# Performance work log

Hardware: AMD Instinct MI355X
Metric: run time of the kernel (lower is better)

## Reference

```python
import jax, jax.numpy as jnp
import numpy as np

N_NODES = 100000


def _gcn_conv(x, W, b, src, dst, deg_inv_sqrt):
    # linear transform first (PyG GCNConv order): [N, F] @ [F, H]
    h = x @ W
    # symmetric normalization per edge: deg^-1/2[src] * deg^-1/2[dst]
    norm = deg_inv_sqrt[src] * deg_inv_sqrt[dst]
    msg = h[src] * norm[:, None]  # [E, H]
    out = jax.ops.segment_sum(msg, dst, num_segments=N_NODES)
    return out + b


def setup_inputs() -> dict:
    key = jax.random.key(0)
    k1, k2, k3, k4 = jax.random.split(key, 4)
    F_IN, H = 512, 512
    E = 800000
    x = jax.random.normal(k1, (N_NODES, F_IN), dtype=jnp.float32)
    edge_index = jax.random.randint(k2, (2, E), 0, N_NODES, dtype=jnp.int64)
    W1 = jax.random.normal(k3, (F_IN, H), dtype=jnp.float32) * (1.0 / np.sqrt(F_IN))
    b1 = jnp.zeros((H,), dtype=jnp.float32)
    W2 = jax.random.normal(k4, (H, H), dtype=jnp.float32) * (1.0 / np.sqrt(H))
    b2 = jnp.zeros((H,), dtype=jnp.float32)
    return {"x": x, "edge_index": edge_index, "W1": W1, "b1": b1, "W2": W2, "b2": b2}


def reference(x, edge_index, W1, b1, W2, b2):
    # add self loops (PyG GCNConv default add_self_loops=True)
    loop = jnp.arange(N_NODES, dtype=edge_index.dtype)
    src = jnp.concatenate([edge_index[0], loop])
    dst = jnp.concatenate([edge_index[1], loop])
    # degree of destination nodes (including self loops)
    deg = jax.ops.segment_sum(jnp.ones_like(dst, dtype=x.dtype), dst, num_segments=N_NODES)
    deg_inv_sqrt = jnp.where(deg > 0, jax.lax.rsqrt(jnp.maximum(deg, 1.0)), 0.0)
    h = jax.nn.relu(_gcn_conv(x, W1, b1, src, dst, deg_inv_sqrt))
    # dropout is identity at inference (training=False)
    out = _gcn_conv(h, W2, b2, src, dst, deg_inv_sqrt)
    return out
```

## Files before the change

kernel.cpp:

```cpp
#include <hip/hip_runtime.h>

#define N_NODES 100000
#define E_EDGES 800000
#define E_TOT   900000
#define F 512

typedef __attribute__((ext_vector_type(8))) short short8;
typedef __attribute__((ext_vector_type(4))) float f32x4;
typedef unsigned int u32;

__device__ __forceinline__ float bfu(unsigned int u) {
    union { unsigned int i; float f; } c; c.i = u << 16; return c.f;
}
__device__ __forceinline__ unsigned short f2b(float f) {
    union { float f; unsigned int u; } c; c.f = f;
    return (unsigned short)((c.u + 0x7fffu + ((c.u >> 16) & 1u)) >> 16);
}
__device__ __forceinline__ float fbits(unsigned int u) {
    union { unsigned int i; float f; } c; c.i = u; return c.f;
}
__device__ __forceinline__ unsigned int bits(float f) {
    union { float f; unsigned int i; } c; c.f = f; return c.i;
}
__device__ __forceinline__ void gload_lds16(const void* g, void* l) {
    __builtin_amdgcn_global_load_lds(
        (const __attribute__((address_space(1))) u32*)g,
        (__attribute__((address_space(3))) u32*)l, 16, 0, 0);
}

__global__ void k_init(unsigned int* deg, unsigned int* counter) {
    int i = blockIdx.x * 256 + threadIdx.x;
    if (i < N_NODES) deg[i] = 1u;
    if (i == 0) *counter = 0u;
}

__global__ void k_hist(const int* __restrict__ ei, unsigned int* deg) {
    int e = blockIdx.x * 256 + threadIdx.x;
    if (e < E_EDGES) atomicAdd(&deg[ei[E_EDGES + e]], 1u);
}

__global__ void k_disalloc(const unsigned int* __restrict__ deg, unsigned int* counter,
                           float* __restrict__ dis,
                           int2* __restrict__ seg, unsigned int* __restrict__ cursor) {
    int i = blockIdx.x * 256 + threadIdx.x;
    if (i < N_NODES) {
        unsigned int d = deg[i];
        dis[i] = rsqrtf((float)d);
        unsigned int p = atomicAdd(counter, d);
        seg[i] = make_int2((int)p, (int)(p + d));
        cursor[i] = p;
    }
}

__global__ void k_scatter(const int* __restrict__ ei, const float* __restrict__ dis,
                          unsigned int* __restrict__ cursor,
                          uint2* __restrict__ ev) {
    int e = blockIdx.x * 256 + threadIdx.x;
    if (e < E_TOT) {
        int s, d;
        if (e < E_EDGES) { s = ei[e]; d = ei[E_EDGES + e]; }
        else             { s = e - E_EDGES; d = s; }
        unsigned int p = atomicAdd(&cursor[d], 1u);
        ev[p] = make_uint2((unsigned)s, bits(dis[s] * dis[d]));
    }
}

__global__ void k_cvtX(const float* __restrict__ xin, unsigned short* __restrict__ xb) {
    int i = blockIdx.x * 256 + threadIdx.x;
    const f32x4* p = (const f32x4*)xin + (size_t)i * 2;
    f32x4 a = __builtin_nontemporal_load(p);
    f32x4 b = __builtin_nontemporal_load(p + 1);
    uint4 o;
    o.x = (unsigned)f2b(a[0]) | ((unsigned)f2b(a[1]) << 16);
    o.y = (unsigned)f2b(a[2]) | ((unsigned)f2b(a[3]) << 16);
    o.z = (unsigned)f2b(b[0]) | ((unsigned)f2b(b[1]) << 16);
    o.w = (unsigned)f2b(b[2]) | ((unsigned)f2b(b[3]) << 16);
    *(uint4*)(xb + (size_t)i * 8) = o;
}

__global__ void k_cvtW(const float* __restrict__ W1, const float* __restrict__ W2,
                       unsigned short* __restrict__ W1t, unsigned short* __restrict__ W2t) {
    int t = blockIdx.x * 256 + threadIdx.x;
    int which = t >= F * F;
    int u = t - which * F * F;
    int n = u >> 9, k = u & 511;
    const float* W = which ? W2 : W1;
    unsigned short* Wt = which ? W2t : W1t;
    Wt[u] = f2b(W[k * F + n]);
}

__global__ __launch_bounds__(512, 2)
void gemm_bt(const unsigned short* __restrict__ A, const unsigned short* __restrict__ Bt,
             const float* __restrict__ bias,
             unsigned short* __restrict__ outb, float* __restrict__ outf,
             int relu, int M) {
    __shared__ unsigned short sm[65536];

    int nwg = gridDim.x * gridDim.y;
    int orig = blockIdx.y * gridDim.x + blockIdx.x;
    int q = nwg >> 3, r = nwg & 7;
    int xcd = orig & 7, j8 = orig >> 3;
    int wgid = (xcd < r ? xcd * (q + 1) : r * (q + 1) + (xcd - r) * q) + j8;
    int by = wgid & 1;
    int bx = wgid >> 1;

    int t  = threadIdx.x;
    int lane = t & 63, w = t >> 6;
    int wr = w >> 2, wc = w & 3;
    int rsel = lane & 15, khalf = (lane >> 4) * 8;

    f32x4 acc[8][4];
    #pragma unroll
    for (int m = 0; m < 8; ++m)
        #pragma unroll
        for (int n = 0; n < 4; ++n)
            acc[m][n] = (f32x4){0.f, 0.f, 0.f, 0.f};

    int rowBase = bx * 256;

    int ar[4], br[4], kcc[4];
    #pragma unroll
    for (int i = 0; i < 4; ++i) {
        int idx = i * 512 + t;
        int rr = idx >> 3;
        kcc[i] = (idx & 7) * 8;
        int ga = rowBase + rr; if (ga >= M) ga = M - 1;
        ar[i] = ga;
        br[i] = by * 256 + rr;
    }

    auto STAGE = [&](int buf, int k0) {
        #pragma unroll
        for (int i = 0; i < 4; ++i) {
            int idx = i * 512 + t;
            gload_lds16(A + (size_t)ar[i] * F + k0 + kcc[i], sm + buf * 16384 + idx * 8);
            gload_lds16(Bt + (size_t)br[i] * F + k0 + kcc[i], sm + 32768 + buf * 16384 + idx * 8);
        }
    };
    auto COMPUTE = [&](int buf) {
        const unsigned short* la = sm + buf * 16384;
        const unsigned short* lb = sm + 32768 + buf * 16384;
        #pragma unroll
        for (int ks = 0; ks < 2; ++ks) {
            int koff = ks * 32 + khalf;
            short8 af[8], bfr[4];
            #pragma unroll
            for (int m = 0; m < 8; ++m)
                af[m] = *(const short8*)&la[(wr * 128 + m * 16 + rsel) * 64 + koff];
            #pragma unroll
            for (int n = 0; n < 4; ++n)
                bfr[n] = *(const short8*)&lb[(wc * 64 + n * 16 + rsel) * 64 + koff];
            #pragma unroll
            for (int m = 0; m < 8; ++m)
                #pragma unroll
                for (int n = 0; n < 4; ++n)
                    acc[m][n] = __builtin_amdgcn_mfma_f32_16x16x32_bf16(af[m], bfr[n], acc[m][n], 0, 0, 0);
        }
    };

    STAGE(0, 0);
    __syncthreads();
    #pragma unroll
    for (int kp = 0; kp < 4; ++kp) {
        STAGE(1, (2 * kp + 1) * 64);
        COMPUTE(0);
        __syncthreads();
        if (kp < 3) STAGE(0, (2 * kp + 2) * 64);
        COMPUTE(1);
        __syncthreads();
    }

    int rq = (lane >> 4) * 4, cq = lane & 15;
    if (outb) {
        #pragma unroll
        for (int m = 0; m < 8; ++m)
            #pragma unroll
            for (int n = 0; n < 4; ++n) {
                int cl = wc * 64 + n * 16 + cq;
                float bv = bias[by * 256 + cl];
                #pragma unroll
                for (int j = 0; j < 4; ++j) {
                    int rl = wr * 128 + m * 16 + rq + j;
                    float v = acc[m][n][j] + bv;
                    if (relu) v = fmaxf(v, 0.f);
                    sm[rl * 256 + cl] = f2b(v);
                }
            }
        __syncthreads();
        #pragma unroll
        for (int p = 0; p < 16; ++p) {
            int sidx = p * 4096 + t * 8;
            int row = sidx >> 8;
            int col = sidx & 255;
            int grow = rowBase + row;
            if (grow < M) {
                uint4 v = *(const uint4*)&sm[sidx];
                *(uint4*)&outb[(size_t)grow * F + by * 256 + col] = v;
            }
        }
    } else {
        #pragma unroll
        for (int m = 0; m < 8; ++m)
            #pragma unroll
            for (int n = 0; n < 4; ++n) {
                int colv = by * 256 + wc * 64 + n * 16 + cq;
                float bv = bias[colv];
                #pragma unroll
                for (int j = 0; j < 4; ++j) {
                    int row = rowBase + wr * 128 + m * 16 + rq + j;
                    if (row < M) {
                        float v = acc[m][n][j] + bv;
                        if (relu) v = fmaxf(v, 0.f);
                        __builtin_nontemporal_store(v, outf + (size_t)row * F + colv);
                    }
                }
            }
    }
}

__global__ __launch_bounds__(256)
void k_agg(const unsigned short* __restrict__ hin, const int2* __restrict__ seg,
           const uint2* __restrict__ ev,
           unsigned short* __restrict__ outb) {
    int node = blockIdx.x * 4 + (threadIdx.x >> 6);
    int lane = threadIdx.x & 63;
    if (node >= N_NODES) return;
    int2 se = seg[node];
    int e0 = se.x, e1 = se.y;
    float acc[8] = {0, 0, 0, 0, 0, 0, 0, 0};
    const unsigned short* base = hin + lane * 8;

    int e = e0;
    int n8 = e0 + ((e1 - e0) & ~7);
    for (; e < n8; e += 8) {
        uint2 p0 = ev[e],     p1 = ev[e + 1], p2 = ev[e + 2], p3 = ev[e + 3];
        uint2 p4 = ev[e + 4], p5 = ev[e + 5], p6 = ev[e + 6], p7 = ev[e + 7];
        uint4 v0 = *(const uint4*)(base + ((size_t)p0.x << 9));
        uint4 v1 = *(const uint4*)(base + ((size_t)p1.x << 9));
        uint4 v2 = *(const uint4*)(base + ((size_t)p2.x << 9));
        uint4 v3 = *(const uint4*)(base + ((size_t)p3.x << 9));
        uint4 v4 = *(const uint4*)(base + ((size_t)p4.x << 9));
        uint4 v5 = *(const uint4*)(base + ((size_t)p5.x << 9));
        uint4 v6 = *(const uint4*)(base + ((size_t)p6.x << 9));
        uint4 v7 = *(const uint4*)(base + ((size_t)p7.x << 9));
        float w0 = fbits(p0.y), w1 = fbits(p1.y), w2 = fbits(p2.y), w3 = fbits(p3.y);
        float w4 = fbits(p4.y), w5 = fbits(p5.y), w6 = fbits(p6.y), w7 = fbits(p7.y);
        acc[0] += w0 * bfu(v0.x & 0xffffu); acc[1] += w0 * bfu(v0.x >> 16);
        acc[2] += w0 * bfu(v0.y & 0xffffu); acc[3] += w0 * bfu(v0.y >> 16);
        acc[4] += w0 * bfu(v0.z & 0xffffu); acc[5] += w0 * bfu(v0.z >> 16);
        acc[6] += w0 * bfu(v0.w & 0xffffu); acc[7] += w0 * bfu(v0.w >> 16);
        acc[0] += w1 * bfu(v1.x & 0xffffu); acc[1] += w1 * bfu(v1.x >> 16);
        acc[2] += w1 * bfu(v1.y & 0xffffu); acc[3] += w1 * bfu(v1.y >> 16);
        acc[4] += w1 * bfu(v1.z & 0xffffu); acc[5] += w1 * bfu(v1.z >> 16);
        acc[6] += w1 * bfu(v1.w & 0xffffu); acc[7] += w1 * bfu(v1.w >> 16);
        acc[0] += w2 * bfu(v2.x & 0xffffu); acc[1] += w2 * bfu(v2.x >> 16);
        acc[2] += w2 * bfu(v2.y & 0xffffu); acc[3] += w2 * bfu(v2.y >> 16);
        acc[4] += w2 * bfu(v2.z & 0xffffu); acc[5] += w2 * bfu(v2.z >> 16);
        acc[6] += w2 * bfu(v2.w & 0xffffu); acc[7] += w2 * bfu(v2.w >> 16);
        acc[0] += w3 * bfu(v3.x & 0xffffu); acc[1] += w3 * bfu(v3.x >> 16);
        acc[2] += w3 * bfu(v3.y & 0xffffu); acc[3] += w3 * bfu(v3.y >> 16);
        acc[4] += w3 * bfu(v3.z & 0xffffu); acc[5] += w3 * bfu(v3.z >> 16);
        acc[6] += w3 * bfu(v3.w & 0xffffu); acc[7] += w3 * bfu(v3.w >> 16);
        acc[0] += w4 * bfu(v4.x & 0xffffu); acc[1] += w4 * bfu(v4.x >> 16);
        acc[2] += w4 * bfu(v4.y & 0xffffu); acc[3] += w4 * bfu(v4.y >> 16);
        acc[4] += w4 * bfu(v4.z & 0xffffu); acc[5] += w4 * bfu(v4.z >> 16);
        acc[6] += w4 * bfu(v4.w & 0xffffu); acc[7] += w4 * bfu(v4.w >> 16);
        acc[0] += w5 * bfu(v5.x & 0xffffu); acc[1] += w5 * bfu(v5.x >> 16);
        acc[2] += w5 * bfu(v5.y & 0xffffu); acc[3] += w5 * bfu(v5.y >> 16);
        acc[4] += w5 * bfu(v5.z & 0xffffu); acc[5] += w5 * bfu(v5.z >> 16);
        acc[6] += w5 * bfu(v5.w & 0xffffu); acc[7] += w5 * bfu(v5.w >> 16);
        acc[0] += w6 * bfu(v6.x & 0xffffu); acc[1] += w6 * bfu(v6.x >> 16);
        acc[2] += w6 * bfu(v6.y & 0xffffu); acc[3] += w6 * bfu(v6.y >> 16);
        acc[4] += w6 * bfu(v6.z & 0xffffu); acc[5] += w6 * bfu(v6.z >> 16);
        acc[6] += w6 * bfu(v6.w & 0xffffu); acc[7] += w6 * bfu(v6.w >> 16);
        acc[0] += w7 * bfu(v7.x & 0xffffu); acc[1] += w7 * bfu(v7.x >> 16);
        acc[2] += w7 * bfu(v7.y & 0xffffu); acc[3] += w7 * bfu(v7.y >> 16);
        acc[4] += w7 * bfu(v7.z & 0xffffu); acc[5] += w7 * bfu(v7.z >> 16);
        acc[6] += w7 * bfu(v7.w & 0xffffu); acc[7] += w7 * bfu(v7.w >> 16);
    }
    for (; e < e1; ++e) {
        uint2 p = ev[e];
        uint4 v = *(const uint4*)(base + ((size_t)p.x << 9));
        float wv = fbits(p.y);
        acc[0] += wv * bfu(v.x & 0xffffu); acc[1] += wv * bfu(v.x >> 16);
        acc[2] += wv * bfu(v.y & 0xffffu); acc[3] += wv * bfu(v.y >> 16);
        acc[4] += wv * bfu(v.z & 0xffffu); acc[5] += wv * bfu(v.z >> 16);
        acc[6] += wv * bfu(v.w & 0xffffu); acc[7] += wv * bfu(v.w >> 16);
    }

    uint4 o;
    o.x = (unsigned)f2b(acc[0]) | ((unsigned)f2b(acc[1]) << 16);
    o.y = (unsigned)f2b(acc[2]) | ((unsigned)f2b(acc[3]) << 16);
    o.z = (unsigned)f2b(acc[4]) | ((unsigned)f2b(acc[5]) << 16);
    o.w = (unsigned)f2b(acc[6]) | ((unsigned)f2b(acc[7]) << 16);
    *(uint4*)(outb + (size_t)node * F + lane * 8) = o;
}

extern "C" void kernel_launch(void* const* d_in, const int* in_sizes, int n_in,
                              void* d_out, int out_size, void* d_ws, size_t ws_size,
                              hipStream_t stream) {
    const float* x  = (const float*)d_in[0];
    const int*   ei = (const int*)d_in[1];
    const float* W1 = (const float*)d_in[2];
    const float* b1 = (const float*)d_in[3];
    const float* W2 = (const float*)d_in[4];
    const float* b2 = (const float*)d_in[5];
    float* out = (float*)d_out;

    char* ws = (char*)d_ws;
    size_t off = 0;
    auto alloc = [&](size_t bytes) -> void* {
        off = (off + 255) & ~(size_t)255;
        void* p = ws + off;
        off += bytes;
        return p;
    };

    unsigned short* tb  = (unsigned short*)alloc((size_t)N_NODES * F * 2);
    unsigned short* W1t = (unsigned short*)alloc((size_t)F * F * 2);
    unsigned short* W2t = (unsigned short*)alloc((size_t)F * F * 2);
    unsigned int*   deg = (unsigned int*)alloc((size_t)N_NODES * 4);
    float*          dis = (float*)alloc((size_t)N_NODES * 4);
    int2*           seg = (int2*)alloc((size_t)N_NODES * 8);
    unsigned int*   cur = (unsigned int*)alloc((size_t)N_NODES * 4);
    unsigned int*   cnt = (unsigned int*)alloc(256);
    uint2*          ev  = (uint2*)alloc((size_t)E_TOT * 8);

    unsigned short* h1b = (unsigned short*)d_out;
    unsigned short* xb  = (unsigned short*)((char*)d_out + (size_t)N_NODES * F * 2);

    int nb = (N_NODES + 255) / 256;

    k_init<<<nb, 256, 0, stream>>>(deg, cnt);
    k_hist<<<(E_EDGES + 255) / 256, 256, 0, stream>>>(ei, deg);
    k_disalloc<<<nb, 256, 0, stream>>>(deg, cnt, dis, seg, cur);
    k_scatter<<<(E_TOT + 255) / 256, 256, 0, stream>>>(ei, dis, cur, ev);

    k_cvtW<<<(2 * F * F) / 256, 256, 0, stream>>>(W1, W2, W1t, W2t);
    k_cvtX<<<(N_NODES * F / 8) / 256, 256, 0, stream>>>(x, xb);

    dim3 ggrid(2, (N_NODES + 255) / 256);

    k_agg<<<(N_NODES + 3) / 4, 256, 0, stream>>>(xb, seg, ev, tb);
    gemm_bt<<<ggrid, 512, 0, stream>>>(tb, W1t, b1, h1b, nullptr, 1, N_NODES);

    k_agg<<<(N_NODES + 3) / 4, 256, 0, stream>>>(h1b, seg, ev, tb);
    gemm_bt<<<ggrid, 512, 0, stream>>>(tb, W2t, b2, nullptr, out, 0, N_NODES);
}
```

Baseline: 647.3 us.

## Bucket each node's CSR edges by source-node chunk to improve gather locality

```diff
diff --git a/kernel.cpp b/kernel.cpp
--- a/kernel.cpp
+++ b/kernel.cpp
@@ -4,6 +4,8 @@
 #define E_EDGES 800000
 #define E_TOT   900000
 #define F 512
+#define NCHUNK 4
+#define CHUNK_SZ 25000
 
 typedef __attribute__((ext_vector_type(8))) short short8;
 typedef __attribute__((ext_vector_type(4))) float f32x4;
@@ -28,39 +30,50 @@
         (__attribute__((address_space(3))) u32*)l, 16, 0, 0);
 }
 
-__global__ void k_init(unsigned int* deg, unsigned int* counter) {
-    int i = blockIdx.x * 256 + threadIdx.x;
-    if (i < N_NODES) deg[i] = 1u;
-    if (i == 0) *counter = 0u;
-}
-
-__global__ void k_hist(const int* __restrict__ ei, unsigned int* deg) {
-    int e = blockIdx.x * 256 + threadIdx.x;
-    if (e < E_EDGES) atomicAdd(&deg[ei[E_EDGES + e]], 1u);
-}
-
-__global__ void k_disalloc(const unsigned int* __restrict__ deg, unsigned int* counter,
-                           float* __restrict__ dis,
-                           int2* __restrict__ seg, unsigned int* __restrict__ cursor) {
+__global__ void k_init(uint4* deg4, unsigned int* counter) {
     int i = blockIdx.x * 256 + threadIdx.x;
     if (i < N_NODES) {
-        unsigned int d = deg[i];
-        dis[i] = rsqrtf((float)d);
-        unsigned int p = atomicAdd(counter, d);
-        seg[i] = make_int2((int)p, (int)(p + d));
-        cursor[i] = p;
+        deg4[i] = make_uint4(0u, 0u, 0u, 0u);
+        ((unsigned int*)deg4)[i * 4 + i / CHUNK_SZ] = 1u;
+    }
+    if (i == 0) *counter = 0u;
+}
+
+__global__ void k_hist(const int* __restrict__ ei, unsigned int* deg4u) {
+    int e = blockIdx.x * 256 + threadIdx.x;
+    if (e < E_EDGES) {
+        int s = ei[e], d = ei[E_EDGES + e];
+        atomicAdd(&deg4u[(size_t)d * 4 + s / CHUNK_SZ], 1u);
+    }
+}
+
+__global__ void k_disalloc(uint4* deg4, unsigned int* counter,
+                           float* __restrict__ dis,
+                           int2* __restrict__ seg, int4* __restrict__ cst) {
+    int i = blockIdx.x * 256 + threadIdx.x;
+    if (i < N_NODES) {
+        uint4 d4 = deg4[i];
+        unsigned int tot = d4.x + d4.y + d4.z + d4.w;
+        dis[i] = rsqrtf((float)tot);
+        unsigned int p = atomicAdd(counter, tot);
+        int4 cs = make_int4((int)p, (int)(p + d4.x),
+                            (int)(p + d4.x + d4.y), (int)(p + d4.x + d4.y + d4.z));
+        cst[i] = cs;
+        seg[i] = make_int2((int)p, (int)(p + tot));
+        deg4[i] = make_uint4((unsigned)cs.x, (unsigned)cs.y,
+                             (unsigned)cs.z, (unsigned)cs.w);
     }
 }
 
 __global__ void k_scatter(const int* __restrict__ ei, const float* __restrict__ dis,
-                          unsigned int* __restrict__ cursor,
+                          unsigned int* __restrict__ cur4,
                           uint2* __restrict__ ev) {
     int e = blockIdx.x * 256 + threadIdx.x;
     if (e < E_TOT) {
         int s, d;
         if (e < E_EDGES) { s = ei[e]; d = ei[E_EDGES + e]; }
         else             { s = e - E_EDGES; d = s; }
-        unsigned int p = atomicAdd(&cursor[d], 1u);
+        unsigned int p = atomicAdd(&cur4[(size_t)d * 4 + s / CHUNK_SZ], 1u);
         ev[p] = make_uint2((unsigned)s, bits(dis[s] * dis[d]));
     }
 }
@@ -218,74 +231,38 @@
     }
 }
 
+#define LOADP(k) uint2 p##k = ev[e + k]
+#define LOADV(k) uint4 v##k = *(const uint4*)(base + ((size_t)p##k.x << 9))
+#define ACCV(k)  { float w_ = fbits(p##k.y); \
+    acc[0] += w_ * bfu(v##k.x & 0xffffu); acc[1] += w_ * bfu(v##k.x >> 16); \
+    acc[2] += w_ * bfu(v##k.y & 0xffffu); acc[3] += w_ * bfu(v##k.y >> 16); \
+    acc[4] += w_ * bfu(v##k.z & 0xffffu); acc[5] += w_ * bfu(v##k.z >> 16); \
+    acc[6] += w_ * bfu(v##k.w & 0xffffu); acc[7] += w_ * bfu(v##k.w >> 16); }
+
 __global__ __launch_bounds__(256)
 void k_agg(const unsigned short* __restrict__ hin, const int2* __restrict__ seg,
-           const uint2* __restrict__ ev,
+           const int4* __restrict__ cst, const uint2* __restrict__ ev,
            unsigned short* __restrict__ outb) {
     int node = blockIdx.x * 4 + (threadIdx.x >> 6);
     int lane = threadIdx.x & 63;
     if (node >= N_NODES) return;
     int2 se = seg[node];
-    int e0 = se.x, e1 = se.y;
+    int4 cs = cst[node];
+    int st[5] = {cs.x, cs.y, cs.z, cs.w, se.y};
     float acc[8] = {0, 0, 0, 0, 0, 0, 0, 0};
     const unsigned short* base = hin + lane * 8;
 
-    int e = e0;
-    int n8 = e0 + ((e1 - e0) & ~7);
-    for (; e < n8; e += 8) {
-        uint2 p0 = ev[e],     p1 = ev[e + 1], p2 = ev[e + 2], p3 = ev[e + 3];
-        uint2 p4 = ev[e + 4], p5 = ev[e + 5], p6 = ev[e + 6], p7 = ev[e + 7];
-        uint4 v0 = *(const uint4*)(base + ((size_t)p0.x << 9));
-        uint4 v1 = *(const uint4*)(base + ((size_t)p1.x << 9));
-        uint4 v2 = *(const uint4*)(base + ((size_t)p2.x << 9));
-        uint4 v3 = *(const uint4*)(base + ((size_t)p3.x << 9));
-        uint4 v4 = *(const uint4*)(base + ((size_t)p4.x << 9));
-        uint4 v5 = *(const uint4*)(base + ((size_t)p5.x << 9));
-        uint4 v6 = *(const uint4*)(base + ((size_t)p6.x << 9));
-        uint4 v7 = *(const uint4*)(base + ((size_t)p7.x << 9));
-        float w0 = fbits(p0.y), w1 = fbits(p1.y), w2 = fbits(p2.y), w3 = fbits(p3.y);
-        float w4 = fbits(p4.y), w5 = fbits(p5.y), w6 = fbits(p6.y), w7 = fbits(p7.y);
-        acc[0] += w0 * bfu(v0.x & 0xffffu); acc[1] += w0 * bfu(v0.x >> 16);
-        acc[2] += w0 * bfu(v0.y & 0xffffu); acc[3] += w0 * bfu(v0.y >> 16);
-        acc[4] += w0 * bfu(v0.z & 0xffffu); acc[5] += w0 * bfu(v0.z >> 16);
-        acc[6] += w0 * bfu(v0.w & 0xffffu); acc[7] += w0 * bfu(v0.w >> 16);
-        acc[0] += w1 * bfu(v1.x & 0xffffu); acc[1] += w1 * bfu(v1.x >> 16);
-        acc[2] += w1 * bfu(v1.y & 0xffffu); acc[3] += w1 * bfu(v1.y >> 16);
-        acc[4] += w1 * bfu(v1.z & 0xffffu); acc[5] += w1 * bfu(v1.z >> 16);
-        acc[6] += w1 * bfu(v1.w & 0xffffu); acc[7] += w1 * bfu(v1.w >> 16);
-        acc[0] += w2 * bfu(v2.x & 0xffffu); acc[1] += w2 * bfu(v2.x >> 16);
-        acc[2] += w2 * bfu(v2.y & 0xffffu); acc[3] += w2 * bfu(v2.y >> 16);
-        acc[4] += w2 * bfu(v2.z & 0xffffu); acc[5] += w2 * bfu(v2.z >> 16);
-        acc[6] += w2 * bfu(v2.w & 0xffffu); acc[7] += w2 * bfu(v2.w >> 16);
-        acc[0] += w3 * bfu(v3.x & 0xffffu); acc[1] += w3 * bfu(v3.x >> 16);
-        acc[2] += w3 * bfu(v3.y & 0xffffu); acc[3] += w3 * bfu(v3.y >> 16);
-        acc[4] += w3 * bfu(v3.z & 0xffffu); acc[5] += w3 * bfu(v3.z >> 16);
-        acc[6] += w3 * bfu(v3.w & 0xffffu); acc[7] += w3 * bfu(v3.w >> 16);
-        acc[0] += w4 * bfu(v4.x & 0xffffu); acc[1] += w4 * bfu(v4.x >> 16);
-        acc[2] += w4 * bfu(v4.y & 0xffffu); acc[3] += w4 * bfu(v4.y >> 16);
-        acc[4] += w4 * bfu(v4.z & 0xffffu); acc[5] += w4 * bfu(v4.z >> 16);
-        acc[6] += w4 * bfu(v4.w & 0xffffu); acc[7] += w4 * bfu(v4.w >> 16);
-        acc[0] += w5 * bfu(v5.x & 0xffffu); acc[1] += w5 * bfu(v5.x >> 16);
-        acc[2] += w5 * bfu(v5.y & 0xffffu); acc[3] += w5 * bfu(v5.y >> 16);
-        acc[4] += w5 * bfu(v5.z & 0xffffu); acc[5] += w5 * bfu(v5.z >> 16);
-        acc[6] += w5 * bfu(v5.w & 0xffffu); acc[7] += w5 * bfu(v5.w >> 16);
-        acc[0] += w6 * bfu(v6.x & 0xffffu); acc[1] += w6 * bfu(v6.x >> 16);
-        acc[2] += w6 * bfu(v6.y & 0xffffu); acc[3] += w6 * bfu(v6.y >> 16);
-        acc[4] += w6 * bfu(v6.z & 0xffffu); acc[5] += w6 * bfu(v6.z >> 16);
-        acc[6] += w6 * bfu(v6.w & 0xffffu); acc[7] += w6 * bfu(v6.w >> 16);
-        acc[0] += w7 * bfu(v7.x & 0xffffu); acc[1] += w7 * bfu(v7.x >> 16);
-        acc[2] += w7 * bfu(v7.y & 0xffffu); acc[3] += w7 * bfu(v7.y >> 16);
-        acc[4] += w7 * bfu(v7.z & 0xffffu); acc[5] += w7 * bfu(v7.z >> 16);
-        acc[6] += w7 * bfu(v7.w & 0xffffu); acc[7] += w7 * bfu(v7.w >> 16);
-    }
-    for (; e < e1; ++e) {
-        uint2 p = ev[e];
-        uint4 v = *(const uint4*)(base + ((size_t)p.x << 9));
-        float wv = fbits(p.y);
-        acc[0] += wv * bfu(v.x & 0xffffu); acc[1] += wv * bfu(v.x >> 16);
-        acc[2] += wv * bfu(v.y & 0xffffu); acc[3] += wv * bfu(v.y >> 16);
-        acc[4] += wv * bfu(v.z & 0xffffu); acc[5] += wv * bfu(v.z >> 16);
-        acc[6] += wv * bfu(v.w & 0xffffu); acc[7] += wv * bfu(v.w >> 16);
+    #pragma unroll
+    for (int c = 0; c < NCHUNK; ++c) {
+        int e = st[c], end = st[c + 1];
+        for (; e + 3 < end; e += 4) {
+            LOADP(0); LOADP(1); LOADP(2); LOADP(3);
+            LOADV(0); LOADV(1); LOADV(2); LOADV(3);
+            ACCV(0); ACCV(1); ACCV(2); ACCV(3);
+        }
+        for (; e < end; ++e) {
+            LOADP(0); LOADV(0); ACCV(0);
+        }
     }
 
     uint4 o;
@@ -316,34 +293,34 @@
         return p;
     };
 
-    unsigned short* tb  = (unsigned short*)alloc((size_t)N_NODES * F * 2);
-    unsigned short* W1t = (unsigned short*)alloc((size_t)F * F * 2);
-    unsigned short* W2t = (unsigned short*)alloc((size_t)F * F * 2);
-    unsigned int*   deg = (unsigned int*)alloc((size_t)N_NODES * 4);
-    float*          dis = (float*)alloc((size_t)N_NODES * 4);
-    int2*           seg = (int2*)alloc((size_t)N_NODES * 8);
-    unsigned int*   cur = (unsigned int*)alloc((size_t)N_NODES * 4);
-    unsigned int*   cnt = (unsigned int*)alloc(256);
-    uint2*          ev  = (uint2*)alloc((size_t)E_TOT * 8);
+    unsigned short* tb   = (unsigned short*)alloc((size_t)N_NODES * F * 2);
+    unsigned short* W1t  = (unsigned short*)alloc((size_t)F * F * 2);
+    unsigned short* W2t  = (unsigned short*)alloc((size_t)F * F * 2);
+    uint4*          deg4 = (uint4*)alloc((size_t)N_NODES * 16);
+    float*          dis  = (float*)alloc((size_t)N_NODES * 4);
+    int2*           seg  = (int2*)alloc((size_t)N_NODES * 8);
+    int4*           cst  = (int4*)alloc((size_t)N_NODES * 16);
+    unsigned int*   cnt  = (unsigned int*)alloc(256);
+    uint2*          ev   = (uint2*)alloc((size_t)E_TOT * 8);
 
     unsigned short* h1b = (unsigned short*)d_out;
     unsigned short* xb  = (unsigned short*)((char*)d_out + (size_t)N_NODES * F * 2);
 
     int nb = (N_NODES + 255) / 256;
 
-    k_init<<<nb, 256, 0, stream>>>(deg, cnt);
-    k_hist<<<(E_EDGES + 255) / 256, 256, 0, stream>>>(ei, deg);
-    k_disalloc<<<nb, 256, 0, stream>>>(deg, cnt, dis, seg, cur);
-    k_scatter<<<(E_TOT + 255) / 256, 256, 0, stream>>>(ei, dis, cur, ev);
+    k_init<<<nb, 256, 0, stream>>>(deg4, cnt);
+    k_hist<<<(E_EDGES + 255) / 256, 256, 0, stream>>>(ei, (unsigned int*)deg4);
+    k_disalloc<<<nb, 256, 0, stream>>>(deg4, cnt, dis, seg, cst);
+    k_scatter<<<(E_TOT + 255) / 256, 256, 0, stream>>>(ei, dis, (unsigned int*)deg4, ev);
 
     k_cvtW<<<(2 * F * F) / 256, 256, 0, stream>>>(W1, W2, W1t, W2t);
     k_cvtX<<<(N_NODES * F / 8) / 256, 256, 0, stream>>>(x, xb);
 
     dim3 ggrid(2, (N_NODES + 255) / 256);
 
-    k_agg<<<(N_NODES + 3) / 4, 256, 0, stream>>>(xb, seg, ev, tb);
+    k_agg<<<(N_NODES + 3) / 4, 256, 0, stream>>>(xb, seg, cst, ev, tb);
     gemm_bt<<<ggrid, 512, 0, stream>>>(tb, W1t, b1, h1b, nullptr, 1, N_NODES);
 
-    k_agg<<<(N_NODES + 3) / 4, 256, 0, stream>>>(h1b, seg, ev, tb);
+    k_agg<<<(N_NODES + 3) / 4, 256, 0, stream>>>(h1b, seg, cst, ev, tb);
     gemm_bt<<<ggrid, 512, 0, stream>>>(tb, W2t, b2, nullptr, out, 0, N_NODES);
 }
```

Result: no change. 639.6 us (-1.2%).

## Restructure GEMM main loop into fine-grained phased pipeline with swizzled LDS

Applied to the files above, without the earlier changes.

```diff
diff --git a/kernel.cpp b/kernel.cpp
--- a/kernel.cpp
+++ b/kernel.cpp
@@ -89,6 +89,47 @@
     Wt[u] = f2b(W[k * F + n]);
 }
 
+
+#define STAGE_CHUNK(BUF, I, K0) { \
+    gload_lds16(A + (size_t)ar[I] * F + (K0) + kcs[I], sm + (BUF) * 16384 + ((I) * 512 + t) * 8); \
+    gload_lds16(Bt + (size_t)br[I] * F + (K0) + kcs[I], sm + 32768 + (BUF) * 16384 + ((I) * 512 + t) * 8); }
+
+#define PHASE(BUF, I, WLIT, DOWAIT, DOSTAGE, K0N) { \
+    if (DOSTAGE) { \
+        STAGE_CHUNK((BUF) ^ 1, 2 * (I), K0N) \
+        STAGE_CHUNK((BUF) ^ 1, 2 * (I) + 1, K0N) \
+    } \
+    if (DOWAIT) { asm volatile("s_waitcnt vmcnt(" #WLIT ")" ::: "memory"); } \
+    __builtin_amdgcn_s_barrier(); \
+    asm volatile("" ::: "memory"); \
+    { \
+        const unsigned short* la = sm + (BUF) * 16384; \
+        const unsigned short* lb = sm + 32768 + (BUF) * 16384; \
+        const int ksq = (I) >> 1, mhq = (I) & 1; \
+        int koff = (ksq * 32 + khalf) ^ kx; \
+        short8 af_[4]; \
+        _Pragma("unroll") \
+        for (int m4 = 0; m4 < 4; ++m4) \
+            af_[m4] = *(const short8*)&la[(wr * 128 + (mhq * 4 + m4) * 16 + rsel) * 64 + koff]; \
+        if (mhq == 0) { \
+            _Pragma("unroll") \
+            for (int n = 0; n < 4; ++n) \
+                bfr[n] = *(const short8*)&lb[(wc * 64 + n * 16 + rsel) * 64 + koff]; \
+        } \
+        __builtin_amdgcn_s_setprio(1); \
+        _Pragma("unroll") \
+        for (int m4 = 0; m4 < 4; ++m4) \
+            _Pragma("unroll") \
+            for (int n = 0; n < 4; ++n) \
+                acc[mhq * 4 + m4][n] = __builtin_amdgcn_mfma_f32_16x16x32_bf16(af_[m4], bfr[n], acc[mhq * 4 + m4][n], 0, 0, 0); \
+        __builtin_amdgcn_s_setprio(0); \
+    } \
+    __builtin_amdgcn_s_barrier(); }
+
+#define KTILE(BUF, K0N) \
+    PHASE(BUF, 0, 4, 1, 1, K0N) PHASE(BUF, 1, 8, 0, 1, K0N) \
+    PHASE(BUF, 2, 8, 0, 0, 0)   PHASE(BUF, 3, 8, 0, 0, 0)
+
 __global__ __launch_bounds__(512, 2)
 void gemm_bt(const unsigned short* __restrict__ A, const unsigned short* __restrict__ Bt,
              const float* __restrict__ bias,
@@ -108,6 +149,7 @@
     int lane = t & 63, w = t >> 6;
     int wr = w >> 2, wc = w & 3;
     int rsel = lane & 15, khalf = (lane >> 4) * 8;
+    int kx = (lane & 4) ? 16 : 0;
 
     f32x4 acc[8][4];
     #pragma unroll
@@ -118,57 +160,26 @@
 
     int rowBase = bx * 256;
 
-    int ar[4], br[4], kcc[4];
+    int ar[4], br[4], kcs[4];
     #pragma unroll
     for (int i = 0; i < 4; ++i) {
         int idx = i * 512 + t;
         int rr = idx >> 3;
-        kcc[i] = (idx & 7) * 8;
+        int kc = (idx & 7) * 8;
+        kcs[i] = kc ^ ((rr & 4) ? 16 : 0);
         int ga = rowBase + rr; if (ga >= M) ga = M - 1;
         ar[i] = ga;
         br[i] = by * 256 + rr;
     }
 
-    auto STAGE = [&](int buf, int k0) {
-        #pragma unroll
-        for (int i = 0; i < 4; ++i) {
-            int idx = i * 512 + t;
-            gload_lds16(A + (size_t)ar[i] * F + k0 + kcc[i], sm + buf * 16384 + idx * 8);
-            gload_lds16(Bt + (size_t)br[i] * F + k0 + kcc[i], sm + 32768 + buf * 16384 + idx * 8);
-        }
-    };
-    auto COMPUTE = [&](int buf) {
-        const unsigned short* la = sm + buf * 16384;
-        const unsigned short* lb = sm + 32768 + buf * 16384;
-        #pragma unroll
-        for (int ks = 0; ks < 2; ++ks) {
-            int koff = ks * 32 + khalf;
-            short8 af[8], bfr[4];
-            #pragma unroll
-            for (int m = 0; m < 8; ++m)
-                af[m] = *(const short8*)&la[(wr * 128 + m * 16 + rsel) * 64 + koff];
-            #pragma unroll
-            for (int n = 0; n < 4; ++n)
-                bfr[n] = *(const short8*)&lb[(wc * 64 + n * 16 + rsel) * 64 + koff];
-            #pragma unroll
-            for (int m = 0; m < 8; ++m)
-                #pragma unroll
-                for (int n = 0; n < 4; ++n)
-                    acc[m][n] = __builtin_amdgcn_mfma_f32_16x16x32_bf16(af[m], bfr[n], acc[m][n], 0, 0, 0);
-        }
-    };
-
-    STAGE(0, 0);
-    __syncthreads();
-    #pragma unroll
-    for (int kp = 0; kp < 4; ++kp) {
-        STAGE(1, (2 * kp + 1) * 64);
-        COMPUTE(0);
-        __syncthreads();
-        if (kp < 3) STAGE(0, (2 * kp + 2) * 64);
-        COMPUTE(1);
-        __syncthreads();
-    }
+    short8 bfr[4];
+
+    STAGE_CHUNK(0, 0, 0) STAGE_CHUNK(0, 1, 0) STAGE_CHUNK(0, 2, 0) STAGE_CHUNK(0, 3, 0)
+
+    KTILE(0,  64) KTILE(1, 128) KTILE(0, 192) KTILE(1, 256)
+    KTILE(0, 320) KTILE(1, 384) KTILE(0, 448)
+    PHASE(1, 0, 0, 1, 0, 0) PHASE(1, 1, 0, 0, 0, 0)
+    PHASE(1, 2, 0, 0, 0, 0) PHASE(1, 3, 0, 0, 0, 0)
 
     int rq = (lane >> 4) * 4, cq = lane & 15;
     if (outb) {
@@ -218,6 +229,14 @@
     }
 }
 
+#define LOADP(k) uint2 p##k = ev[e + k]
+#define LOADV(k) uint4 v##k = *(const uint4*)(base + ((size_t)p##k.x << 9))
+#define ACCV(k)  { float w_ = fbits(p##k.y); \
+    acc[0] += w_ * bfu(v##k.x & 0xffffu); acc[1] += w_ * bfu(v##k.x >> 16); \
+    acc[2] += w_ * bfu(v##k.y & 0xffffu); acc[3] += w_ * bfu(v##k.y >> 16); \
+    acc[4] += w_ * bfu(v##k.z & 0xffffu); acc[5] += w_ * bfu(v##k.z >> 16); \
+    acc[6] += w_ * bfu(v##k.w & 0xffffu); acc[7] += w_ * bfu(v##k.w >> 16); }
+
 __global__ __launch_bounds__(256)
 void k_agg(const unsigned short* __restrict__ hin, const int2* __restrict__ seg,
            const uint2* __restrict__ ev,
@@ -233,59 +252,15 @@
     int e = e0;
     int n8 = e0 + ((e1 - e0) & ~7);
     for (; e < n8; e += 8) {
-        uint2 p0 = ev[e],     p1 = ev[e + 1], p2 = ev[e + 2], p3 = ev[e + 3];
-        uint2 p4 = ev[e + 4], p5 = ev[e + 5], p6 = ev[e + 6], p7 = ev[e + 7];
-        uint4 v0 = *(const uint4*)(base + ((size_t)p0.x << 9));
-        uint4 v1 = *(const uint4*)(base + ((size_t)p1.x << 9));
-        uint4 v2 = *(const uint4*)(base + ((size_t)p2.x << 9));
-        uint4 v3 = *(const uint4*)(base + ((size_t)p3.x << 9));
-        uint4 v4 = *(const uint4*)(base + ((size_t)p4.x << 9));
-        uint4 v5 = *(const uint4*)(base + ((size_t)p5.x << 9));
-        uint4 v6 = *(const uint4*)(base + ((size_t)p6.x << 9));
-        uint4 v7 = *(const uint4*)(base + ((size_t)p7.x << 9));
-        float w0 = fbits(p0.y), w1 = fbits(p1.y), w2 = fbits(p2.y), w3 = fbits(p3.y);
-        float w4 = fbits(p4.y), w5 = fbits(p5.y), w6 = fbits(p6.y), w7 = fbits(p7.y);
-        acc[0] += w0 * bfu(v0.x & 0xffffu); acc[1] += w0 * bfu(v0.x >> 16);
-        acc[2] += w0 * bfu(v0.y & 0xffffu); acc[3] += w0 * bfu(v0.y >> 16);
-        acc[4] += w0 * bfu(v0.z & 0xffffu); acc[5] += w0 * bfu(v0.z >> 16);
-        acc[6] += w0 * bfu(v0.w & 0xffffu); acc[7] += w0 * bfu(v0.w >> 16);
-        acc[0] += w1 * bfu(v1.x & 0xffffu); acc[1] += w1 * bfu(v1.x >> 16);
-        acc[2] += w1 * bfu(v1.y & 0xffffu); acc[3] += w1 * bfu(v1.y >> 16);
-        acc[4] += w1 * bfu(v1.z & 0xffffu); acc[5] += w1 * bfu(v1.z >> 16);
-        acc[6] += w1 * bfu(v1.w & 0xffffu); acc[7] += w1 * bfu(v1.w >> 16);
-        acc[0] += w2 * bfu(v2.x & 0xffffu); acc[1] += w2 * bfu(v2.x >> 16);
-        acc[2] += w2 * bfu(v2.y & 0xffffu); acc[3] += w2 * bfu(v2.y >> 16);
-        acc[4] += w2 * bfu(v2.z & 0xffffu); acc[5] += w2 * bfu(v2.z >> 16);
-        acc[6] += w2 * bfu(v2.w & 0xffffu); acc[7] += w2 * bfu(v2.w >> 16);
-        acc[0] += w3 * bfu(v3.x & 0xffffu); acc[1] += w3 * bfu(v3.x >> 16);
-        acc[2] += w3 * bfu(v3.y & 0xffffu); acc[3] += w3 * bfu(v3.y >> 16);
-        acc[4] += w3 * bfu(v3.z & 0xffffu); acc[5] += w3 * bfu(v3.z >> 16);
-        acc[6] += w3 * bfu(v3.w & 0xffffu); acc[7] += w3 * bfu(v3.w >> 16);
-        acc[0] += w4 * bfu(v4.x & 0xffffu); acc[1] += w4 * bfu(v4.x >> 16);
-        acc[2] += w4 * bfu(v4.y & 0xffffu); acc[3] += w4 * bfu(v4.y >> 16);
-        acc[4] += w4 * bfu(v4.z & 0xffffu); acc[5] += w4 * bfu(v4.z >> 16);
-        acc[6] += w4 * bfu(v4.w & 0xffffu); acc[7] += w4 * bfu(v4.w >> 16);
-        acc[0] += w5 * bfu(v5.x & 0xffffu); acc[1] += w5 * bfu(v5.x >> 16);
-        acc[2] += w5 * bfu(v5.y & 0xffffu); acc[3] += w5 * bfu(v5.y >> 16);
-        acc[4] += w5 * bfu(v5.z & 0xffffu); acc[5] += w5 * bfu(v5.z >> 16);
-        acc[6] += w5 * bfu(v5.w & 0xffffu); acc[7] += w5 * bfu(v5.w >> 16);
-        acc[0] += w6 * bfu(v6.x & 0xffffu); acc[1] += w6 * bfu(v6.x >> 16);
-        acc[2] += w6 * bfu(v6.y & 0xffffu); acc[3] += w6 * bfu(v6.y >> 16);
-        acc[4] += w6 * bfu(v6.z & 0xffffu); acc[5] += w6 * bfu(v6.z >> 16);
-        acc[6] += w6 * bfu(v6.w & 0xffffu); acc[7] += w6 * bfu(v6.w >> 16);
-        acc[0] += w7 * bfu(v7.x & 0xffffu); acc[1] += w7 * bfu(v7.x >> 16);
-        acc[2] += w7 * bfu(v7.y & 0xffffu); acc[3] += w7 * bfu(v7.y >> 16);
-        acc[4] += w7 * bfu(v7.z & 0xffffu); acc[5] += w7 * bfu(v7.z >> 16);
-        acc[6] += w7 * bfu(v7.w & 0xffffu); acc[7] += w7 * bfu(v7.w >> 16);
+        LOADP(0); LOADP(1); LOADP(2); LOADP(3);
+        LOADP(4); LOADP(5); LOADP(6); LOADP(7);
+        LOADV(0); LOADV(1); LOADV(2); LOADV(3);
+        LOADV(4); LOADV(5); LOADV(6); LOADV(7);
+        ACCV(0); ACCV(1); ACCV(2); ACCV(3);
+        ACCV(4); ACCV(5); ACCV(6); ACCV(7);
     }
     for (; e < e1; ++e) {
-        uint2 p = ev[e];
-        uint4 v = *(const uint4*)(base + ((size_t)p.x << 9));
-        float wv = fbits(p.y);
-        acc[0] += wv * bfu(v.x & 0xffffu); acc[1] += wv * bfu(v.x >> 16);
-        acc[2] += wv * bfu(v.y & 0xffffu); acc[3] += wv * bfu(v.y >> 16);
-        acc[4] += wv * bfu(v.z & 0xffffu); acc[5] += wv * bfu(v.z >> 16);
-        acc[6] += wv * bfu(v.w & 0xffffu); acc[7] += wv * bfu(v.w >> 16);
+        LOADP(0); LOADV(0); ACCV(0);
     }
 
     uint4 o;
```

Measured after the change: 645.7 us. No clear change (-0.2%).
